# Performance work log

Measured on AMD Instinct MI355X. Metric: run time of the kernel, lower is better.

## Reference

```python
import jax, jax.numpy as jnp
import numpy as np

DIM = 1024
HEADS = 16
DIM_HEAD = 64
INNER = HEADS * DIM_HEAD  # 1024
SCALE = DIM_HEAD ** -0.5


def setup_inputs() -> dict:
    key = jax.random.key(0)
    k1, k2, k3, k4 = jax.random.split(key, 4)
    B, N = 2, 2048
    x = jax.random.normal(k1, (B, N, DIM), dtype=jnp.float32)
    # to_qkv: Linear(dim, 3*inner_dim, bias=False); weight stored as [out, in] in torch,
    # here as [in, out] for x @ W.
    w_qkv = jax.random.normal(k2, (DIM, 3 * INNER), dtype=jnp.float32) * (DIM ** -0.5)
    # to_out: Linear(inner_dim, dim) with bias
    w_out = jax.random.normal(k3, (INNER, DIM), dtype=jnp.float32) * (INNER ** -0.5)
    b_out = jax.random.normal(k4, (DIM,), dtype=jnp.float32) * 0.02
    return {"x": x, "w_qkv": w_qkv, "w_out": w_out, "b_out": b_out}


def reference(x, w_qkv, w_out, b_out):
    B, N, _ = x.shape
    qkv = x @ w_qkv                                  # [B, N, 3*INNER]
    q, k, v = jnp.split(qkv, 3, axis=-1)             # each [B, N, INNER]
    def to_heads(t):
        return t.reshape(B, N, HEADS, DIM_HEAD).transpose(0, 2, 1, 3)  # [B,H,N,D]
    q, k, v = to_heads(q), to_heads(k), to_heads(v)
    dots = jnp.einsum('bhnd,bhmd->bhnm', q, k) * SCALE  # [B,H,N,N]
    attn = jax.nn.softmax(dots, axis=-1)
    out = jnp.einsum('bhnm,bhmd->bhnd', attn, v)        # [B,H,N,D]
    out = out.transpose(0, 2, 1, 3).reshape(B, N, INNER)
    return out @ w_out + b_out
```

## Files before the change

kernel.cpp:

```cpp
#include <hip/hip_runtime.h>
#include <hip/hip_bf16.h>
#include <stdint.h>

#define PDIM   1024
#define HEADS  16
#define DHEAD  64
#define BATCH  2
#define SEQ    2048
#define ROWS   (BATCH*SEQ)
#define NBH    (BATCH*HEADS)

typedef __attribute__((ext_vector_type(8))) short s8v;
typedef __attribute__((ext_vector_type(4))) float f32x4;
typedef unsigned short ushort_t;
typedef unsigned int   uint32;

#define QSCALE 0.18033688011112042f
#define MFIX 12.0f

__device__ __forceinline__ ushort_t f2bf(float x){
  union { float f; uint32 u; } v; v.f = x;
  uint32 r = v.u + 0x7FFFu + ((v.u >> 16) & 1u);
  return (ushort_t)(r >> 16);
}
__device__ __forceinline__ ushort_t f2bf_trunc(float x){
  union { float f; uint32 u; } v; v.f = x;
  return (ushort_t)(v.u >> 16);
}

typedef const __attribute__((address_space(1))) void* gas_ptr;
typedef __attribute__((address_space(3))) void*       las_ptr;
__device__ __forceinline__ void g2l16(const void* g, void* l){
  __builtin_amdgcn_global_load_lds((gas_ptr)g, (las_ptr)l, 16, 0, 0);
}

__global__ __launch_bounds__(256) void k_cvt(const float* __restrict__ src,
                                             ushort_t* __restrict__ dst, int n4){
  int i = blockIdx.x * 256 + threadIdx.x;
  if (i >= n4) return;
  float4 v = reinterpret_cast<const float4*>(src)[i];
  reinterpret_cast<ushort4*>(dst)[i] =
      make_ushort4(f2bf(v.x), f2bf(v.y), f2bf(v.z), f2bf(v.w));
}

__global__ __launch_bounds__(256) void k_tcvt(const float* __restrict__ src, int R, int C,
                                              ushort_t* __restrict__ dh){
  __shared__ float tile[64][65];
  int cb = blockIdx.x * 64, rb = blockIdx.y * 64;
  int t = threadIdx.x;
  int lw = t >> 6;
  int lc = t & 63;
#pragma unroll
  for (int i = 0; i < 16; i++){
    int r = i * 4 + lw;
    tile[r][lc] = src[(size_t)(rb + r) * C + cb + lc];
  }
  __syncthreads();
#pragma unroll
  for (int i = 0; i < 16; i++){
    int c = i * 4 + lw;
    dh[(size_t)(cb + c) * R + rb + lc] = f2bf(tile[lc][c]);
  }
}

#define GBM 128
#define GBN 128
#define GBK 64

__global__ __launch_bounds__(256, 2) void k_gemm_qkv(
    const ushort_t* __restrict__ Xh, const ushort_t* __restrict__ Wqt_h,
    ushort_t* __restrict__ Qh, ushort_t* __restrict__ Kh, ushort_t* __restrict__ Vth){
  __shared__ __align__(16) ushort_t Asm[2][GBM * GBK];
  __shared__ __align__(16) ushort_t Bsm[2][GBM * GBK];
  const int tid  = threadIdx.x;
  const int wave = tid >> 6, lane = tid & 63;
  const int mb = blockIdx.y * GBM, nb = blockIdx.x * GBN;
  const int wr = wave >> 1, wc = wave & 1;
  const int l15 = lane & 15, l4 = lane >> 4;
  const int rsub = lane >> 3;
  const int schunk = ((lane & 7) ^ rsub) * 8;
  f32x4 acc[4][4] = {};

  auto stage = [&](int buf, int kb){
    int k0 = kb * GBK;
#pragma unroll
    for (int i = 0; i < 4; i++){
      int row = (i * 4 + wave) * 8 + rsub;
      g2l16(Xh    + (size_t)(mb + row) * 1024 + k0 + schunk, &Asm[buf][(i * 4 + wave) * 512]);
      g2l16(Wqt_h + (size_t)(nb + row) * 1024 + k0 + schunk, &Bsm[buf][(i * 4 + wave) * 512]);
    }
  };

  stage(0, 0);

  for (int kb = 0; kb < 16; kb++){
    const int cur = kb & 1;
    if (kb < 15){
      stage(cur ^ 1, kb + 1);
      asm volatile("s_waitcnt vmcnt(8)" ::: "memory");
    } else {
      asm volatile("s_waitcnt vmcnt(0)" ::: "memory");
    }
    __builtin_amdgcn_s_barrier();
    __builtin_amdgcn_s_setprio(1);
#pragma unroll
    for (int ks = 0; ks < 2; ks++){
      s8v af[4], bfr[4];
#pragma unroll
      for (int f = 0; f < 4; f++){
        int ch = (((ks * 4 + l4) ^ (l15 & 7)) << 3);
        af[f]  = *reinterpret_cast<const s8v*>(&Asm[cur][(wr * 64 + f * 16 + l15) * 64 + ch]);
        bfr[f] = *reinterpret_cast<const s8v*>(&Bsm[cur][(wc * 64 + f * 16 + l15) * 64 + ch]);
      }
#pragma unroll
      for (int fr = 0; fr < 4; fr++)
#pragma unroll
        for (int fc = 0; fc < 4; fc++)
          acc[fr][fc] = __builtin_amdgcn_mfma_f32_16x16x32_bf16(af[fr], bfr[fc], acc[fr][fc], 0, 0, 0);
    }
    __builtin_amdgcn_s_setprio(0);
    __builtin_amdgcn_s_barrier();
  }

  const int pnum = nb >> 10;
#pragma unroll
  for (int fr = 0; fr < 4; fr++){
    int row  = mb + wr * 64 + fr * 16 + l4 * 4;
    int b    = row >> 11;
    int nseq = row & 2047;
#pragma unroll
    for (int fc = 0; fc < 4; fc++){
      int col = nb + wc * 64 + fc * 16 + l15;
      int rem = col & 1023;
      int h = rem >> 6, d = rem & 63;
      int bh = b * 16 + h;
      if (pnum == 0){
        size_t base = ((size_t)bh * SEQ + nseq) * 64 + d;
#pragma unroll
        for (int r = 0; r < 4; r++)
          Qh[base + (size_t)r * 64] = f2bf(acc[fr][fc][r] * QSCALE);
      } else if (pnum == 1){
        size_t base = ((size_t)bh * SEQ + nseq) * 64 + d;
#pragma unroll
        for (int r = 0; r < 4; r++)
          Kh[base + (size_t)r * 64] = f2bf(acc[fr][fc][r]);
      } else {
        size_t base = ((size_t)bh * 64 + d) * SEQ + nseq;
        *reinterpret_cast<ushort4*>(&Vth[base]) =
            make_ushort4(f2bf(acc[fr][fc][0]), f2bf(acc[fr][fc][1]),
                         f2bf(acc[fr][fc][2]), f2bf(acc[fr][fc][3]));
      }
    }
  }
}

__global__ __launch_bounds__(256, 2) void k_gemm_out(
    const ushort_t* __restrict__ Ah, const ushort_t* __restrict__ Bth,
    float* __restrict__ C, const float* __restrict__ bias){
  __shared__ __align__(16) ushort_t Asm[2][GBM * GBK];
  __shared__ __align__(16) ushort_t Bsm[2][GBM * GBK];
  const int tid  = threadIdx.x;
  const int wave = tid >> 6, lane = tid & 63;
  const int mb = blockIdx.y * GBM, nb = blockIdx.x * GBN;
  const int wr = wave >> 1, wc = wave & 1;
  const int l15 = lane & 15, l4 = lane >> 4;
  const int rsub = lane >> 3;
  const int schunk = ((lane & 7) ^ rsub) * 8;
  f32x4 acc[4][4] = {};

  auto stage = [&](int buf, int kb){
    int k0 = kb * GBK;
#pragma unroll
    for (int i = 0; i < 4; i++){
      int row = (i * 4 + wave) * 8 + rsub;
      g2l16(Ah  + (size_t)(mb + row) * 1024 + k0 + schunk, &Asm[buf][(i * 4 + wave) * 512]);
      g2l16(Bth + (size_t)(nb + row) * 1024 + k0 + schunk, &Bsm[buf][(i * 4 + wave) * 512]);
    }
  };

  stage(0, 0);

  for (int kb = 0; kb < 16; kb++){
    const int cur = kb & 1;
    if (kb < 15){
      stage(cur ^ 1, kb + 1);
      asm volatile("s_waitcnt vmcnt(8)" ::: "memory");
    } else {
      asm volatile("s_waitcnt vmcnt(0)" ::: "memory");
    }
    __builtin_amdgcn_s_barrier();
    __builtin_amdgcn_s_setprio(1);
#pragma unroll
    for (int ks = 0; ks < 2; ks++){
      s8v af[4], bfr[4];
#pragma unroll
      for (int f = 0; f < 4; f++){
        int ch = (((ks * 4 + l4) ^ (l15 & 7)) << 3);
        af[f]  = *reinterpret_cast<const s8v*>(&Asm[cur][(wr * 64 + f * 16 + l15) * 64 + ch]);
        bfr[f] = *reinterpret_cast<const s8v*>(&Bsm[cur][(wc * 64 + f * 16 + l15) * 64 + ch]);
      }
#pragma unroll
      for (int fr = 0; fr < 4; fr++)
#pragma unroll
        for (int fc = 0; fc < 4; fc++)
          acc[fr][fc] = __builtin_amdgcn_mfma_f32_16x16x32_bf16(af[fr], bfr[fc], acc[fr][fc], 0, 0, 0);
    }
    __builtin_amdgcn_s_setprio(0);
    __builtin_amdgcn_s_barrier();
  }
#pragma unroll
  for (int fr = 0; fr < 4; fr++){
    int row = mb + wr * 64 + fr * 16 + l4 * 4;
#pragma unroll
    for (int fc = 0; fc < 4; fc++){
      int col = nb + wc * 64 + fc * 16 + l15;
      float bv = bias[col];
#pragma unroll
      for (int r = 0; r < 4; r++)
        C[(size_t)(row + r) * 1024 + col] = acc[fr][fc][r] + bv;
    }
  }
}

__global__ __launch_bounds__(256, 4) void k_flash(
    const ushort_t* __restrict__ Qh, const ushort_t* __restrict__ Kh,
    const ushort_t* __restrict__ Vth, ushort_t* __restrict__ Ah){
  __shared__ __align__(16) ushort_t KhS[2][64 * 64];
  __shared__ __align__(16) ushort_t VhS[64 * 64];
  __shared__ __align__(16) ushort_t PhS[64 * 72];
  const int lid = blockIdx.x;
  const int xcd = lid & 7, g = lid >> 3;
  const int bh = xcd * 4 + (g & 3);
  const int qb = (g >> 2) * 64;
  const int tid = threadIdx.x, wave = tid >> 6, lane = tid & 63;
  const int l15 = lane & 15, l4 = lane >> 4;
  const int b = bh >> 4, h = bh & 15;
  const size_t hbase = (size_t)bh * SEQ * 64;
  const int rsub = lane >> 3;
  const int schunk = ((lane & 7) ^ rsub) * 8;

  s8v qhf[2];
#pragma unroll
  for (int ks = 0; ks < 2; ks++){
    size_t off = hbase + (size_t)(qb + wave * 16 + l15) * 64 + ks * 32 + l4 * 8;
    qhf[ks] = *reinterpret_cast<const s8v*>(&Qh[off]);
  }

  f32x4 o[4] = {};
  float lsum[4] = {};

  auto stageK = [&](int buf, int kt){
    int kvb = kt * 64;
#pragma unroll
    for (int i = 0; i < 2; i++){
      int row = (i * 4 + wave) * 8 + rsub;
      g2l16(Kh + hbase + (size_t)(kvb + row) * 64 + schunk, &KhS[buf][(i * 4 + wave) * 512]);
    }
  };
  auto stageV = [&](int kt){
    int kvb = kt * 64;
#pragma unroll
    for (int i = 0; i < 2; i++){
      int row = (i * 4 + wave) * 8 + rsub;
      g2l16(Vth + ((size_t)bh * 64 + row) * SEQ + kvb + schunk, &VhS[(i * 4 + wave) * 512]);
    }
  };

  stageK(0, 0);

  for (int kt = 0; kt < 32; kt++){
    const int cur = kt & 1;
    stageV(kt);
    if (kt < 31){
      stageK(cur ^ 1, kt + 1);
      asm volatile("s_waitcnt vmcnt(4)" ::: "memory");
    } else {
      asm volatile("s_waitcnt vmcnt(2)" ::: "memory");
    }
    __builtin_amdgcn_s_barrier();

    f32x4 s[4] = {};
    __builtin_amdgcn_s_setprio(1);
#pragma unroll
    for (int ks = 0; ks < 2; ks++)
#pragma unroll
      for (int fc = 0; fc < 4; fc++){
        int rK = fc * 16 + l15;
        int ch = ((ks * 4 + l4) ^ (rK & 7)) << 3;
        s8v kh = *reinterpret_cast<const s8v*>(&KhS[cur][rK * 64 + ch]);
        s[fc] = __builtin_amdgcn_mfma_f32_16x16x32_bf16(qhf[ks], kh, s[fc], 0, 0, 0);
      }
    __builtin_amdgcn_s_setprio(0);

#pragma unroll
    for (int fc = 0; fc < 4; fc++)
#pragma unroll
      for (int r = 0; r < 4; r++){
        float p = __builtin_amdgcn_exp2f(s[fc][r] - MFIX);
        lsum[r] += p;
        int prow = wave * 16 + l4 * 4 + r;
        int col  = (fc * 16 + l15) ^ (((prow >> 2) & 3) << 3);
        PhS[prow * 72 + col] = f2bf_trunc(p);
      }

    if (kt < 31){
      asm volatile("s_waitcnt vmcnt(2)" ::: "memory");
    } else {
      asm volatile("s_waitcnt vmcnt(0)" ::: "memory");
    }
    __builtin_amdgcn_s_barrier();

    __builtin_amdgcn_s_setprio(1);
#pragma unroll
    for (int c = 0; c < 2; c++){
      int prow = wave * 16 + l15;
      int u = (prow >> 2) & 3;
      s8v pa = *reinterpret_cast<const s8v*>(&PhS[prow * 72 + (((c * 4 + l4) ^ u) << 3)]);
#pragma unroll
      for (int fd = 0; fd < 4; fd++){
        int rV = fd * 16 + l15;
        int ch = ((c * 4 + l4) ^ (rV & 7)) << 3;
        s8v vh = *reinterpret_cast<const s8v*>(&VhS[rV * 64 + ch]);
        o[fd] = __builtin_amdgcn_mfma_f32_16x16x32_bf16(pa, vh, o[fd], 0, 0, 0);
      }
    }
    __builtin_amdgcn_s_setprio(0);
    __builtin_amdgcn_s_barrier();
  }

#pragma unroll
  for (int msk = 1; msk < 16; msk <<= 1)
#pragma unroll
    for (int r = 0; r < 4; r++)
      lsum[r] += __shfl_xor(lsum[r], msk);
#pragma unroll
  for (int r = 0; r < 4; r++){
    float inv = 1.f / lsum[r];
    int n = qb + wave * 16 + l4 * 4 + r;
    size_t rowbase = (size_t)(b * SEQ + n) * 1024 + h * 64;
#pragma unroll
    for (int fd = 0; fd < 4; fd++)
      Ah[rowbase + fd * 16 + l15] = f2bf(o[fd][r] * inv);
  }
}

extern "C" void kernel_launch(void* const* d_in, const int* in_sizes, int n_in,
                              void* d_out, int out_size, void* d_ws, size_t ws_size,
                              hipStream_t stream){
  const float* x     = (const float*)d_in[0];
  const float* w_qkv = (const float*)d_in[1];
  const float* w_out = (const float*)d_in[2];
  const float* b_out = (const float*)d_in[3];
  float* out = (float*)d_out;
  char* ws = (char*)d_ws;

  ushort_t* Xh    = (ushort_t*)(ws);
  ushort_t* Wqt_h = (ushort_t*)(ws + 8388608);
  ushort_t* Wot_h = (ushort_t*)(ws + 14680064);
  ushort_t* Qh    = (ushort_t*)(ws + 16777216);
  ushort_t* Kh    = (ushort_t*)(ws + 25165824);
  ushort_t* Vth   = (ushort_t*)(ws + 33554432);
  ushort_t* Ah    = (ushort_t*)(ws + 41943040);

  k_cvt<<<4096, 256, 0, stream>>>(x, Xh, ROWS * PDIM / 4);
  k_tcvt<<<dim3(48, 16), 256, 0, stream>>>(w_qkv, 1024, 3072, Wqt_h);
  k_tcvt<<<dim3(16, 16), 256, 0, stream>>>(w_out, 1024, 1024, Wot_h);
  k_gemm_qkv<<<dim3(24, 32), 256, 0, stream>>>(Xh, Wqt_h, Qh, Kh, Vth);
  k_flash<<<1024, 256, 0, stream>>>(Qh, Kh, Vth, Ah);
  k_gemm_out<<<dim3(8, 32), 256, 0, stream>>>(Ah, Wot_h, out, b_out);
}
```

Before: 133.6 us.

## Transpose QK MFMA output so each lane holds one query row and packs P stores

Swaps the MFMA operands so the score tile is computed transposed, giving each lane a single query row with four consecutive keys. This lets the P tile be written to LDS as packed bf16 pairs using v_cvt_pk_bf16_f32 in 8-byte stores instead of 16 scalar 2-byte stores, and collapses the per-row sum to one scalar needing only two cross-lane shuffles. The LDS layout and swizzle of P and the read side are changed to match. The conversion now rounds rather than truncates, and the final normalization uses a shuffle to fetch each row's sum.

```diff
diff --git a/kernel.cpp b/kernel.cpp
--- a/kernel.cpp
+++ b/kernel.cpp
@@ -23,9 +23,10 @@
   uint32 r = v.u + 0x7FFFu + ((v.u >> 16) & 1u);
   return (ushort_t)(r >> 16);
 }
-__device__ __forceinline__ ushort_t f2bf_trunc(float x){
-  union { float f; uint32 u; } v; v.f = x;
-  return (ushort_t)(v.u >> 16);
+__device__ __forceinline__ uint32 cvt_pk_bf16(float lo, float hi){
+  uint32 r;
+  asm("v_cvt_pk_bf16_f32 %0, %1, %2" : "=v"(r) : "v"(lo), "v"(hi));
+  return r;
 }
 
 typedef const __attribute__((address_space(1))) void* gas_ptr;
@@ -238,6 +239,8 @@
   const size_t hbase = (size_t)bh * SEQ * 64;
   const int rsub = lane >> 3;
   const int schunk = ((lane & 7) ^ rsub) * 8;
+  const int prow  = wave * 16 + l15;
+  const int pkey  = l15 & 3;
 
   s8v qhf[2];
 #pragma unroll
@@ -247,7 +250,7 @@
   }
 
   f32x4 o[4] = {};
-  float lsum[4] = {};
+  float lsum = 0.f;
 
   auto stageK = [&](int buf, int kt){
     int kvb = kt * 64;
@@ -288,20 +291,22 @@
         int rK = fc * 16 + l15;
         int ch = ((ks * 4 + l4) ^ (rK & 7)) << 3;
         s8v kh = *reinterpret_cast<const s8v*>(&KhS[cur][rK * 64 + ch]);
-        s[fc] = __builtin_amdgcn_mfma_f32_16x16x32_bf16(qhf[ks], kh, s[fc], 0, 0, 0);
+        s[fc] = __builtin_amdgcn_mfma_f32_16x16x32_bf16(kh, qhf[ks], s[fc], 0, 0, 0);
       }
     __builtin_amdgcn_s_setprio(0);
 
 #pragma unroll
-    for (int fc = 0; fc < 4; fc++)
-#pragma unroll
-      for (int r = 0; r < 4; r++){
-        float p = __builtin_amdgcn_exp2f(s[fc][r] - MFIX);
-        lsum[r] += p;
-        int prow = wave * 16 + l4 * 4 + r;
-        int col  = (fc * 16 + l15) ^ (((prow >> 2) & 3) << 3);
-        PhS[prow * 72 + col] = f2bf_trunc(p);
-      }
+    for (int fc = 0; fc < 4; fc++){
+      float p0 = __builtin_amdgcn_exp2f(s[fc][0] - MFIX);
+      float p1 = __builtin_amdgcn_exp2f(s[fc][1] - MFIX);
+      float p2 = __builtin_amdgcn_exp2f(s[fc][2] - MFIX);
+      float p3 = __builtin_amdgcn_exp2f(s[fc][3] - MFIX);
+      lsum += (p0 + p1) + (p2 + p3);
+      uint2 w;
+      w.x = cvt_pk_bf16(p0, p1);
+      w.y = cvt_pk_bf16(p2, p3);
+      *reinterpret_cast<uint2*>(&PhS[prow * 72 + ((fc ^ pkey) << 4) + (l4 << 2)]) = w;
+    }
 
     if (kt < 31){
       asm volatile("s_waitcnt vmcnt(2)" ::: "memory");
@@ -313,9 +318,8 @@
     __builtin_amdgcn_s_setprio(1);
 #pragma unroll
     for (int c = 0; c < 2; c++){
-      int prow = wave * 16 + l15;
-      int u = (prow >> 2) & 3;
-      s8v pa = *reinterpret_cast<const s8v*>(&PhS[prow * 72 + (((c * 4 + l4) ^ u) << 3)]);
+      int gidx = (2 * c + (l4 >> 1)) ^ pkey;
+      s8v pa = *reinterpret_cast<const s8v*>(&PhS[prow * 72 + (gidx << 4) + ((l4 & 1) << 3)]);
 #pragma unroll
       for (int fd = 0; fd < 4; fd++){
         int rV = fd * 16 + l15;
@@ -328,14 +332,11 @@
     __builtin_amdgcn_s_barrier();
   }
 
-#pragma unroll
-  for (int msk = 1; msk < 16; msk <<= 1)
-#pragma unroll
-    for (int r = 0; r < 4; r++)
-      lsum[r] += __shfl_xor(lsum[r], msk);
+  lsum += __shfl_xor(lsum, 16);
+  lsum += __shfl_xor(lsum, 32);
 #pragma unroll
   for (int r = 0; r < 4; r++){
-    float inv = 1.f / lsum[r];
+    float inv = 1.f / __shfl(lsum, l4 * 4 + r);
     int n = qb + wave * 16 + l4 * 4 + r;
     size_t rowbase = (size_t)(b * SEQ + n) * 1024 + h * 64;
 #pragma unroll
```

Result: faster. 127.9 us (-4.3%).
